# Performance work log

Measured on AMD Instinct MI355X. Metric: run time of the kernel, lower is better.

Reference implementation:

```python
import jax, jax.numpy as jnp
import numpy as np

# irreps layout: 256x0e (dim 256) + 128x1o (dim 384) + 64x2e (dim 320) -> total 960
MULS = (256, 128, 64)
DIMS = (1, 3, 5)  # 2l+1 for l = 0, 1, 2


def setup_inputs() -> dict:
    key = jax.random.key(0)
    k0, k1, k2, k3 = jax.random.split(key, 4)
    N = 131072
    total = sum(m * d for m, d in zip(MULS, DIMS))  # 960
    return {
        "features": jax.random.normal(k0, (N, total), dtype=jnp.float32),
        "w0": jax.random.normal(k1, (256, 256), dtype=jnp.float32),
        "w1": jax.random.normal(k2, (128, 128), dtype=jnp.float32),
        "w2": jax.random.normal(k3, (64, 64), dtype=jnp.float32),
    }


def _linear_irreps(features, weights):
    # Equivariant Linear == block-diagonal per-irrep matmul over the multiplicity
    # axis, broadcast over the (2l+1) m-components, scaled by 1/sqrt(mul_in)
    # (the net of e3nn's path_weight sqrt((2l+1)/mul_in) and the w3j 1/sqrt(2l+1)).
    outs = []
    off = 0
    for w, mul, d in zip(weights, MULS, DIMS):
        x = features[:, off:off + mul * d].reshape(-1, mul, d)  # [N, u, i]
        scale = 1.0 / np.sqrt(mul).astype(np.float32)
        y = jnp.einsum('zui,uw->zwi', x, w) * scale  # [N, w, i]
        outs.append(y.reshape(y.shape[0], mul * d))
        off += mul * d
    return jnp.concatenate(outs, axis=-1)  # [N, 960]


def reference(features, w0, w1, w2):
    return _linear_irreps(features, (w0, w1, w2))
```

## Files before the change

### kernel.cpp

```cpp
#include <hip/hip_runtime.h>

typedef short bf16x8 __attribute__((ext_vector_type(8)));
typedef float f32x4 __attribute__((ext_vector_type(4)));

__device__ __forceinline__ unsigned short f2bf(float f) {
    union { float f; unsigned u; } a;
    a.f = f;
    unsigned u = a.u;
    u += 0x7fffu + ((u >> 16) & 1u);
    return (unsigned short)(u >> 16);
}

__global__ void convert_w(const float* __restrict__ w, unsigned short* __restrict__ wt,
                          int mul, float scale) {
    int idx = blockIdx.x * blockDim.x + threadIdx.x;
    if (idx >= mul * mul) return;
    int n = idx / mul;
    int k = idx % mul;
    wt[idx] = f2bf(w[k * mul + n] * scale);
}

template<int MUL, int D, int OFF, int GM, int GN>
__global__ __launch_bounds__(256)
void irreps_linear(const float* __restrict__ x, const unsigned short* __restrict__ wt,
                   float* __restrict__ out) {
    constexpr int BM     = 32;
    constexpr int MP     = BM * D;
    constexpr int MT     = MP / 16;
    constexpr int NTL    = MUL / 16;
    constexpr int WM     = MT / GM;
    constexpr int WN     = NTL / GN;
    constexpr int LDA    = MUL + 8;
    constexpr int KSTEPS = MUL / 32;
    constexpr int REG    = MUL * D;
    constexpr int W4     = REG / 4;
    constexpr int LDC    = MUL + 1;
    constexpr int ABYTES = MP * LDA * 2;
    constexpr int CBYTES = (D > 1) ? MP * LDC * 4 : 0;
    constexpr int SBYTES = ABYTES > CBYTES ? ABYTES : CBYTES;

    __shared__ __align__(16) char smem[SBYTES];
    unsigned short* As = (unsigned short*)smem;

    const int  tid = threadIdx.x;
    const long z0  = (long)blockIdx.x * BM;
    const float* xr   = x   + z0 * 960 + OFF;
    float*       orow = out + z0 * 960 + OFF;

    #pragma unroll
    for (int it = 0; it < (BM * W4) / 256; ++it) {
        int idx = tid + it * 256;
        int zl  = idx / W4;
        int c4  = (idx % W4) * 4;
        f32x4 v = *(const f32x4*)(xr + (long)zl * 960 + c4);
        #pragma unroll
        for (int e = 0; e < 4; ++e) {
            int c = c4 + e;
            As[(zl * D + (c % D)) * LDA + (c / D)] = f2bf(v[e]);
        }
    }
    __syncthreads();

    const int lane = tid & 63;
    const int wv   = tid >> 6;
    const int wm0  = (wv / GN) * WM;
    const int wn0  = (wv % GN) * WN;
    const int lr   = lane & 15;
    const int lk   = (lane >> 4) * 8;

    f32x4 acc[WM][WN] = {};
    #pragma unroll
    for (int ks = 0; ks < KSTEPS; ++ks) {
        const int k0 = ks * 32 + lk;
        bf16x8 bfr[WN];
        #pragma unroll
        for (int in = 0; in < WN; ++in)
            bfr[in] = *(const bf16x8*)(wt + ((wn0 + in) * 16 + lr) * MUL + k0);
        #pragma unroll
        for (int im = 0; im < WM; ++im) {
            bf16x8 afr = *(const bf16x8*)(As + ((wm0 + im) * 16 + lr) * LDA + k0);
            #pragma unroll
            for (int in = 0; in < WN; ++in)
                acc[im][in] = __builtin_amdgcn_mfma_f32_16x16x32_bf16(
                    afr, bfr[in], acc[im][in], 0, 0, 0);
        }
    }

    if constexpr (D == 1) {
        #pragma unroll
        for (int im = 0; im < WM; ++im) {
            #pragma unroll
            for (int in = 0; in < WN; ++in) {
                int n  = (wn0 + in) * 16 + lr;
                int mb = (wm0 + im) * 16 + (lane >> 4) * 4;
                #pragma unroll
                for (int j = 0; j < 4; ++j)
                    orow[(long)(mb + j) * 960 + n] = acc[im][in][j];
            }
        }
    } else {
        __syncthreads();
        float* Cs = (float*)smem;
        #pragma unroll
        for (int im = 0; im < WM; ++im) {
            #pragma unroll
            for (int in = 0; in < WN; ++in) {
                int n  = (wn0 + in) * 16 + lr;
                int mb = (wm0 + im) * 16 + (lane >> 4) * 4;
                #pragma unroll
                for (int j = 0; j < 4; ++j)
                    Cs[(mb + j) * LDC + n] = acc[im][in][j];
            }
        }
        __syncthreads();
        #pragma unroll
        for (int it = 0; it < (BM * W4) / 256; ++it) {
            int idx = tid + it * 256;
            int zl  = idx / W4;
            int c4  = (idx % W4) * 4;
            f32x4 v;
            #pragma unroll
            for (int e = 0; e < 4; ++e) {
                int c = c4 + e;
                v[e] = Cs[(zl * D + (c % D)) * LDC + (c / D)];
            }
            *(f32x4*)(orow + (long)zl * 960 + c4) = v;
        }
    }
}

extern "C" void kernel_launch(void* const* d_in, const int* in_sizes, int n_in,
                              void* d_out, int out_size, void* d_ws, size_t ws_size,
                              hipStream_t stream) {
    const float* x  = (const float*)d_in[0];
    const float* w0 = (const float*)d_in[1];
    const float* w1 = (const float*)d_in[2];
    const float* w2 = (const float*)d_in[3];
    float* out = (float*)d_out;
    unsigned short* wt = (unsigned short*)d_ws;

    const int N  = in_sizes[0] / 960;
    const int nb = N / 32;

    convert_w<<<(256 * 256) / 256, 256, 0, stream>>>(w0, wt,         256, 0.0625f);
    convert_w<<<(128 * 128) / 256, 256, 0, stream>>>(w1, wt + 65536, 128, 0.08838834764831845f);
    convert_w<<<( 64 *  64) / 256, 256, 0, stream>>>(w2, wt + 81920,  64, 0.125f);

    irreps_linear<256, 1,   0, 1, 4><<<nb, 256, 0, stream>>>(x, wt,         out);
    irreps_linear<128, 3, 256, 2, 2><<<nb, 256, 0, stream>>>(x, wt + 65536, out);
    irreps_linear< 64, 5, 640, 2, 2><<<nb, 256, 0, stream>>>(x, wt + 81920, out);
}
```

Before: 307.9 us.

## Fuse three per-irrep GEMM kernels into one kernel over full rows

Replaces the three separate per-irrep kernel launches with one 512-thread kernel. Each block loads a full contiguous 960-float row tile once, scatters it into three bf16 LDS tiles, runs all three MFMA GEMMs, and writes the outputs back through LDS staged in sequence. This removes the extra launches and turns the strided partial-row reads into fully contiguous loads. In exchange it needs about 66KB of LDS and more syncs per block, which limits occupancy.

```diff
diff --git a/kernel.cpp b/kernel.cpp
--- a/kernel.cpp
+++ b/kernel.cpp
@@ -9,6 +9,10 @@
     unsigned u = a.u;
     u += 0x7fffu + ((u >> 16) & 1u);
     return (unsigned short)(u >> 16);
+}
+
+__device__ __forceinline__ f32x4 mfma16(bf16x8 a, bf16x8 b, f32x4 c) {
+    return __builtin_amdgcn_mfma_f32_16x16x32_bf16(a, b, c, 0, 0, 0);
 }
 
 __global__ void convert_w(const float* __restrict__ w, unsigned short* __restrict__ wt,
@@ -20,112 +24,167 @@
     wt[idx] = f2bf(w[k * mul + n] * scale);
 }
 
-template<int MUL, int D, int OFF, int GM, int GN>
-__global__ __launch_bounds__(256)
-void irreps_linear(const float* __restrict__ x, const unsigned short* __restrict__ wt,
-                   float* __restrict__ out) {
-    constexpr int BM     = 32;
-    constexpr int MP     = BM * D;
-    constexpr int MT     = MP / 16;
-    constexpr int NTL    = MUL / 16;
-    constexpr int WM     = MT / GM;
-    constexpr int WN     = NTL / GN;
-    constexpr int LDA    = MUL + 8;
-    constexpr int KSTEPS = MUL / 32;
-    constexpr int REG    = MUL * D;
-    constexpr int W4     = REG / 4;
-    constexpr int LDC    = MUL + 1;
-    constexpr int ABYTES = MP * LDA * 2;
-    constexpr int CBYTES = (D > 1) ? MP * LDC * 4 : 0;
-    constexpr int SBYTES = ABYTES > CBYTES ? ABYTES : CBYTES;
-
-    __shared__ __align__(16) char smem[SBYTES];
-    unsigned short* As = (unsigned short*)smem;
+__global__ __launch_bounds__(512, 4)
+void fused_linear(const float* __restrict__ x, const unsigned short* __restrict__ wt,
+                  float* __restrict__ out) {
+    __shared__ __align__(16) char smem[66048];
+    unsigned short* As0 = (unsigned short*)smem;
+    unsigned short* As1 = As0 + 32 * 264;
+    unsigned short* As2 = As1 + 96 * 136;
+    float* Cs = (float*)smem;
 
     const int  tid = threadIdx.x;
-    const long z0  = (long)blockIdx.x * BM;
-    const float* xr   = x   + z0 * 960 + OFF;
-    float*       orow = out + z0 * 960 + OFF;
-
-    #pragma unroll
-    for (int it = 0; it < (BM * W4) / 256; ++it) {
-        int idx = tid + it * 256;
-        int zl  = idx / W4;
-        int c4  = (idx % W4) * 4;
-        f32x4 v = *(const f32x4*)(xr + (long)zl * 960 + c4);
+    const long z0  = (long)blockIdx.x * 32;
+    const float* xr   = x   + z0 * 960;
+    float*       orow = out + z0 * 960;
+
+    #pragma unroll
+    for (int it = 0; it < 15; ++it) {
+        int idx = tid + it * 512;
+        f32x4 v = *(const f32x4*)(xr + (long)idx * 4);
+        int zl = idx / 240;
+        int c4 = (idx % 240) * 4;
         #pragma unroll
         for (int e = 0; e < 4; ++e) {
             int c = c4 + e;
-            As[(zl * D + (c % D)) * LDA + (c / D)] = f2bf(v[e]);
+            unsigned short b = f2bf(v[e]);
+            if (c < 256) {
+                As0[zl * 264 + c] = b;
+            } else if (c < 640) {
+                int cc = c - 256;
+                As1[(zl * 3 + cc % 3) * 136 + cc / 3] = b;
+            } else {
+                int cc = c - 640;
+                As2[(zl * 5 + cc % 5) * 72 + cc / 5] = b;
+            }
         }
     }
     __syncthreads();
 
     const int lane = tid & 63;
     const int wv   = tid >> 6;
-    const int wm0  = (wv / GN) * WM;
-    const int wn0  = (wv % GN) * WN;
     const int lr   = lane & 15;
-    const int lk   = (lane >> 4) * 8;
-
-    f32x4 acc[WM][WN] = {};
-    #pragma unroll
-    for (int ks = 0; ks < KSTEPS; ++ks) {
-        const int k0 = ks * 32 + lk;
-        bf16x8 bfr[WN];
-        #pragma unroll
-        for (int in = 0; in < WN; ++in)
-            bfr[in] = *(const bf16x8*)(wt + ((wn0 + in) * 16 + lr) * MUL + k0);
-        #pragma unroll
-        for (int im = 0; im < WM; ++im) {
-            bf16x8 afr = *(const bf16x8*)(As + ((wm0 + im) * 16 + lr) * LDA + k0);
-            #pragma unroll
-            for (int in = 0; in < WN; ++in)
-                acc[im][in] = __builtin_amdgcn_mfma_f32_16x16x32_bf16(
-                    afr, bfr[in], acc[im][in], 0, 0, 0);
-        }
-    }
-
-    if constexpr (D == 1) {
-        #pragma unroll
-        for (int im = 0; im < WM; ++im) {
-            #pragma unroll
-            for (int in = 0; in < WN; ++in) {
-                int n  = (wn0 + in) * 16 + lr;
-                int mb = (wm0 + im) * 16 + (lane >> 4) * 4;
-                #pragma unroll
-                for (int j = 0; j < 4; ++j)
-                    orow[(long)(mb + j) * 960 + n] = acc[im][in][j];
-            }
-        }
-    } else {
-        __syncthreads();
-        float* Cs = (float*)smem;
-        #pragma unroll
-        for (int im = 0; im < WM; ++im) {
-            #pragma unroll
-            for (int in = 0; in < WN; ++in) {
-                int n  = (wn0 + in) * 16 + lr;
-                int mb = (wm0 + im) * 16 + (lane >> 4) * 4;
-                #pragma unroll
-                for (int j = 0; j < 4; ++j)
-                    Cs[(mb + j) * LDC + n] = acc[im][in][j];
-            }
-        }
-        __syncthreads();
-        #pragma unroll
-        for (int it = 0; it < (BM * W4) / 256; ++it) {
-            int idx = tid + it * 256;
-            int zl  = idx / W4;
-            int c4  = (idx % W4) * 4;
-            f32x4 v;
-            #pragma unroll
-            for (int e = 0; e < 4; ++e) {
-                int c = c4 + e;
-                v[e] = Cs[(zl * D + (c % D)) * LDC + (c / D)];
-            }
-            *(f32x4*)(orow + (long)zl * 960 + c4) = v;
-        }
+    const int q    = lane >> 4;
+    const int lk   = q * 8;
+
+    f32x4 acc0[2][2] = {};
+    {
+        const unsigned short* w0 = wt;
+        #pragma unroll
+        for (int ks = 0; ks < 8; ++ks) {
+            int k0 = ks * 32 + lk;
+            bf16x8 b0 = *(const bf16x8*)(w0 + ((wv * 2 + 0) * 16 + lr) * 256 + k0);
+            bf16x8 b1 = *(const bf16x8*)(w0 + ((wv * 2 + 1) * 16 + lr) * 256 + k0);
+            #pragma unroll
+            for (int im = 0; im < 2; ++im) {
+                bf16x8 a = *(const bf16x8*)(As0 + (im * 16 + lr) * 264 + k0);
+                acc0[im][0] = mfma16(a, b0, acc0[im][0]);
+                acc0[im][1] = mfma16(a, b1, acc0[im][1]);
+            }
+        }
+    }
+
+    const int r1 = wv >> 2, c1 = wv & 3;
+    f32x4 acc1[3][2] = {};
+    {
+        const unsigned short* w1 = wt + 65536;
+        #pragma unroll
+        for (int ks = 0; ks < 4; ++ks) {
+            int k0 = ks * 32 + lk;
+            bf16x8 b0 = *(const bf16x8*)(w1 + ((c1 * 2 + 0) * 16 + lr) * 128 + k0);
+            bf16x8 b1 = *(const bf16x8*)(w1 + ((c1 * 2 + 1) * 16 + lr) * 128 + k0);
+            #pragma unroll
+            for (int im = 0; im < 3; ++im) {
+                bf16x8 a = *(const bf16x8*)(As1 + ((r1 * 3 + im) * 16 + lr) * 136 + k0);
+                acc1[im][0] = mfma16(a, b0, acc1[im][0]);
+                acc1[im][1] = mfma16(a, b1, acc1[im][1]);
+            }
+        }
+    }
+
+    f32x4 acc2[5] = {};
+    {
+        const unsigned short* w2 = wt + 81920;
+        #pragma unroll
+        for (int ks = 0; ks < 2; ++ks) {
+            int k0 = ks * 32 + lk;
+            bf16x8 b0 = *(const bf16x8*)(w2 + (c1 * 16 + lr) * 64 + k0);
+            #pragma unroll
+            for (int im = 0; im < 5; ++im) {
+                bf16x8 a = *(const bf16x8*)(As2 + ((r1 * 5 + im) * 16 + lr) * 72 + k0);
+                acc2[im] = mfma16(a, b0, acc2[im]);
+            }
+        }
+    }
+    __syncthreads();
+
+    #pragma unroll
+    for (int im = 0; im < 2; ++im)
+        #pragma unroll
+        for (int in = 0; in < 2; ++in) {
+            int col = (wv * 2 + in) * 16 + lr;
+            int row = im * 16 + q * 4;
+            #pragma unroll
+            for (int j = 0; j < 4; ++j)
+                Cs[(row + j) * 257 + col] = acc0[im][in][j];
+        }
+    __syncthreads();
+    #pragma unroll
+    for (int it = 0; it < 4; ++it) {
+        int idx = tid + it * 512;
+        int zl = idx / 64, c4 = (idx % 64) * 4;
+        f32x4 v;
+        #pragma unroll
+        for (int e = 0; e < 4; ++e) v[e] = Cs[zl * 257 + c4 + e];
+        *(f32x4*)(orow + (long)zl * 960 + c4) = v;
+    }
+    __syncthreads();
+
+    #pragma unroll
+    for (int im = 0; im < 3; ++im)
+        #pragma unroll
+        for (int in = 0; in < 2; ++in) {
+            int col = (c1 * 2 + in) * 16 + lr;
+            int row = (r1 * 3 + im) * 16 + q * 4;
+            #pragma unroll
+            for (int j = 0; j < 4; ++j)
+                Cs[(row + j) * 129 + col] = acc1[im][in][j];
+        }
+    __syncthreads();
+    #pragma unroll
+    for (int it = 0; it < 6; ++it) {
+        int idx = tid + it * 512;
+        int zl = idx / 96, c4 = (idx % 96) * 4;
+        f32x4 v;
+        #pragma unroll
+        for (int e = 0; e < 4; ++e) {
+            int c = c4 + e;
+            v[e] = Cs[(zl * 3 + c % 3) * 129 + c / 3];
+        }
+        *(f32x4*)(orow + (long)zl * 960 + 256 + c4) = v;
+    }
+    __syncthreads();
+
+    #pragma unroll
+    for (int im = 0; im < 5; ++im) {
+        int col = c1 * 16 + lr;
+        int row = (r1 * 5 + im) * 16 + q * 4;
+        #pragma unroll
+        for (int j = 0; j < 4; ++j)
+            Cs[(row + j) * 65 + col] = acc2[im][j];
+    }
+    __syncthreads();
+    #pragma unroll
+    for (int it = 0; it < 5; ++it) {
+        int idx = tid + it * 512;
+        int zl = idx / 80, c4 = (idx % 80) * 4;
+        f32x4 v;
+        #pragma unroll
+        for (int e = 0; e < 4; ++e) {
+            int c = c4 + e;
+            v[e] = Cs[(zl * 5 + c % 5) * 65 + c / 5];
+        }
+        *(f32x4*)(orow + (long)zl * 960 + 640 + c4) = v;
     }
 }
 
@@ -146,7 +205,5 @@
     convert_w<<<(128 * 128) / 256, 256, 0, stream>>>(w1, wt + 65536, 128, 0.08838834764831845f);
     convert_w<<<( 64 *  64) / 256, 256, 0, stream>>>(w2, wt + 81920,  64, 0.125f);
 
-    irreps_linear<256, 1,   0, 1, 4><<<nb, 256, 0, stream>>>(x, wt,         out);
-    irreps_linear<128, 3, 256, 2, 2><<<nb, 256, 0, stream>>>(x, wt + 65536, out);
-    irreps_linear< 64, 5, 640, 2, 2><<<nb, 256, 0, stream>>>(x, wt + 81920, out);
-}
+    fused_linear<<<nb, 512, 0, stream>>>(x, wt, out);
+}
```

After: 296.7 us. -3.7%, faster.

## Fuse irreps into one kernel using Kronecker-expanded block-diagonal weights

Applied to the files above, without the earlier changes.

Expands each l>0 weight into a dense (mul*D)x(mul*D) matrix that is zero except where the m-components match. This lets the input be loaded contiguously without the per-component transpose through shared memory. All three irreps are then processed in a single 512-thread kernel over 64-row tiles, replacing three launches. The trade-off is extra wasted MFMA work: about three times the FLOPs for l=1 and five times for l=2. Weight reads from global memory also grow.

```diff
diff --git a/kernel.cpp b/kernel.cpp
--- a/kernel.cpp
+++ b/kernel.cpp
@@ -4,129 +4,115 @@
 typedef float f32x4 __attribute__((ext_vector_type(4)));
 
 __device__ __forceinline__ unsigned short f2bf(float f) {
-    union { float f; unsigned u; } a;
-    a.f = f;
+    union { float f; unsigned u; } a; a.f = f;
     unsigned u = a.u;
     u += 0x7fffu + ((u >> 16) & 1u);
     return (unsigned short)(u >> 16);
 }
 
-__global__ void convert_w(const float* __restrict__ w, unsigned short* __restrict__ wt,
-                          int mul, float scale) {
-    int idx = blockIdx.x * blockDim.x + threadIdx.x;
-    if (idx >= mul * mul) return;
-    int n = idx / mul;
-    int k = idx % mul;
-    wt[idx] = f2bf(w[k * mul + n] * scale);
+__device__ __forceinline__ f32x4 mfma16(bf16x8 a, bf16x8 b, f32x4 c) {
+    return __builtin_amdgcn_mfma_f32_16x16x32_bf16(a, b, c, 0, 0, 0);
 }
 
-template<int MUL, int D, int OFF, int GM, int GN>
-__global__ __launch_bounds__(256)
-void irreps_linear(const float* __restrict__ x, const unsigned short* __restrict__ wt,
-                   float* __restrict__ out) {
-    constexpr int BM     = 32;
-    constexpr int MP     = BM * D;
-    constexpr int MT     = MP / 16;
-    constexpr int NTL    = MUL / 16;
-    constexpr int WM     = MT / GM;
-    constexpr int WN     = NTL / GN;
-    constexpr int LDA    = MUL + 8;
-    constexpr int KSTEPS = MUL / 32;
-    constexpr int REG    = MUL * D;
-    constexpr int W4     = REG / 4;
-    constexpr int LDC    = MUL + 1;
-    constexpr int ABYTES = MP * LDA * 2;
-    constexpr int CBYTES = (D > 1) ? MP * LDC * 4 : 0;
-    constexpr int SBYTES = ABYTES > CBYTES ? ABYTES : CBYTES;
+template<int D, int MUL>
+__global__ void expand_w(const float* __restrict__ w, unsigned short* __restrict__ wt,
+                         float scale) {
+    const int n = blockIdx.x;
+    const int k = threadIdx.x;
+    float v = 0.0f;
+    if (D == 1 || (n % D) == (k % D))
+        v = w[(k / D) * MUL + (n / D)] * scale;
+    wt[n * (MUL * D) + k] = f2bf(v);
+}
 
-    __shared__ __align__(16) char smem[SBYTES];
-    unsigned short* As = (unsigned short*)smem;
-
-    const int  tid = threadIdx.x;
-    const long z0  = (long)blockIdx.x * BM;
-    const float* xr   = x   + z0 * 960 + OFF;
-    float*       orow = out + z0 * 960 + OFF;
+template<int KP, int OFF, int BASE, bool TAIL>
+__device__ __forceinline__ void do_block(const float* __restrict__ xr,
+                                         const unsigned short* __restrict__ wb,
+                                         float* __restrict__ orow,
+                                         unsigned short* As,
+                                         int tid, int wv, int lr, int q) {
+    constexpr int P     = KP + 8;
+    constexpr int KS    = KP / 32;
+    constexpr int C8    = KP / 8;
+    constexpr int ITERS = KP / 64;
+    constexpr int NTW   = TAIL ? 3 : BASE;
 
     #pragma unroll
-    for (int it = 0; it < (BM * W4) / 256; ++it) {
-        int idx = tid + it * 256;
-        int zl  = idx / W4;
-        int c4  = (idx % W4) * 4;
-        f32x4 v = *(const f32x4*)(xr + (long)zl * 960 + c4);
-        #pragma unroll
-        for (int e = 0; e < 4; ++e) {
-            int c = c4 + e;
-            As[(zl * D + (c % D)) * LDA + (c / D)] = f2bf(v[e]);
-        }
+    for (int it = 0; it < ITERS; ++it) {
+        int idx = tid + it * 512;
+        int zl  = idx / C8;
+        int c8  = (idx - zl * C8) * 8;
+        const float* p = xr + zl * 960 + OFF + c8;
+        f32x4 v0 = *(const f32x4*)p;
+        f32x4 v1 = *(const f32x4*)(p + 4);
+        bf16x8 sv;
+        sv[0] = f2bf(v0[0]); sv[1] = f2bf(v0[1]); sv[2] = f2bf(v0[2]); sv[3] = f2bf(v0[3]);
+        sv[4] = f2bf(v1[0]); sv[5] = f2bf(v1[1]); sv[6] = f2bf(v1[2]); sv[7] = f2bf(v1[3]);
+        *(bf16x8*)(As + zl * P + c8) = sv;
     }
     __syncthreads();
 
-    const int lane = tid & 63;
-    const int wv   = tid >> 6;
-    const int wm0  = (wv / GN) * WM;
-    const int wn0  = (wv % GN) * WN;
-    const int lr   = lane & 15;
-    const int lk   = (lane >> 4) * 8;
+    int nts[NTW];
+    #pragma unroll
+    for (int in = 0; in < NTW; ++in)
+        nts[in] = (!TAIL || in < 2) ? (wv * BASE + in) : (16 + wv);
+    const bool t3 = !TAIL || (wv < 4);
 
-    f32x4 acc[WM][WN] = {};
+    f32x4 acc[4][NTW];
     #pragma unroll
-    for (int ks = 0; ks < KSTEPS; ++ks) {
-        const int k0 = ks * 32 + lk;
-        bf16x8 bfr[WN];
+    for (int mt = 0; mt < 4; ++mt)
         #pragma unroll
-        for (int in = 0; in < WN; ++in)
-            bfr[in] = *(const bf16x8*)(wt + ((wn0 + in) * 16 + lr) * MUL + k0);
+        for (int in = 0; in < NTW; ++in)
+            acc[mt][in] = (f32x4){0.f, 0.f, 0.f, 0.f};
+
+    #pragma unroll
+    for (int ks = 0; ks < KS; ++ks) {
+        const int kb = ks * 32 + q * 8;
+        bf16x8 b[NTW];
         #pragma unroll
-        for (int im = 0; im < WM; ++im) {
-            bf16x8 afr = *(const bf16x8*)(As + ((wm0 + im) * 16 + lr) * LDA + k0);
+        for (int in = 0; in < NTW; ++in)
+            if (in < 2 || t3)
+                b[in] = *(const bf16x8*)(wb + (nts[in] * 16 + lr) * KP + kb);
+        #pragma unroll
+        for (int mt = 0; mt < 4; ++mt) {
+            bf16x8 a = *(const bf16x8*)(As + (mt * 16 + lr) * P + kb);
             #pragma unroll
-            for (int in = 0; in < WN; ++in)
-                acc[im][in] = __builtin_amdgcn_mfma_f32_16x16x32_bf16(
-                    afr, bfr[in], acc[im][in], 0, 0, 0);
+            for (int in = 0; in < NTW; ++in)
+                if (in < 2 || t3)
+                    acc[mt][in] = mfma16(a, b[in], acc[mt][in]);
         }
     }
 
-    if constexpr (D == 1) {
+    #pragma unroll
+    for (int mt = 0; mt < 4; ++mt)
         #pragma unroll
-        for (int im = 0; im < WM; ++im) {
-            #pragma unroll
-            for (int in = 0; in < WN; ++in) {
-                int n  = (wn0 + in) * 16 + lr;
-                int mb = (wm0 + im) * 16 + (lane >> 4) * 4;
+        for (int in = 0; in < NTW; ++in)
+            if (in < 2 || t3) {
+                const int col = OFF + nts[in] * 16 + lr;
                 #pragma unroll
                 for (int j = 0; j < 4; ++j)
-                    orow[(long)(mb + j) * 960 + n] = acc[im][in][j];
+                    orow[(mt * 16 + q * 4 + j) * 960 + col] = acc[mt][in][j];
             }
-        }
-    } else {
-        __syncthreads();
-        float* Cs = (float*)smem;
-        #pragma unroll
-        for (int im = 0; im < WM; ++im) {
-            #pragma unroll
-            for (int in = 0; in < WN; ++in) {
-                int n  = (wn0 + in) * 16 + lr;
-                int mb = (wm0 + im) * 16 + (lane >> 4) * 4;
-                #pragma unroll
-                for (int j = 0; j < 4; ++j)
-                    Cs[(mb + j) * LDC + n] = acc[im][in][j];
-            }
-        }
-        __syncthreads();
-        #pragma unroll
-        for (int it = 0; it < (BM * W4) / 256; ++it) {
-            int idx = tid + it * 256;
-            int zl  = idx / W4;
-            int c4  = (idx % W4) * 4;
-            f32x4 v;
-            #pragma unroll
-            for (int e = 0; e < 4; ++e) {
-                int c = c4 + e;
-                v[e] = Cs[(zl * D + (c % D)) * LDC + (c / D)];
-            }
-            *(f32x4*)(orow + (long)zl * 960 + c4) = v;
-        }
-    }
+}
+
+__global__ __launch_bounds__(512, 4)
+void fused_linear(const float* __restrict__ x, const unsigned short* __restrict__ wt,
+                  float* __restrict__ out) {
+    __shared__ __align__(16) unsigned short As[64 * 392];
+    const int tid  = threadIdx.x;
+    const int lane = tid & 63;
+    const int wv   = tid >> 6;
+    const int lr   = lane & 15;
+    const int q    = lane >> 4;
+    const long z0  = (long)blockIdx.x * 64;
+    const float* xr = x + z0 * 960;
+    float* orow = out + z0 * 960;
+
+    do_block<256,   0, 2, false>(xr, wt,          orow, As, tid, wv, lr, q);
+    __syncthreads();
+    do_block<384, 256, 3, false>(xr, wt +  65536, orow, As, tid, wv, lr, q);
+    __syncthreads();
+    do_block<320, 640, 2, true >(xr, wt + 212992, orow, As, tid, wv, lr, q);
 }
 
 extern "C" void kernel_launch(void* const* d_in, const int* in_sizes, int n_in,
@@ -139,14 +125,11 @@
     float* out = (float*)d_out;
     unsigned short* wt = (unsigned short*)d_ws;
 
-    const int N  = in_sizes[0] / 960;
-    const int nb = N / 32;
+    const int N = in_sizes[0] / 960;
 
-    convert_w<<<(256 * 256) / 256, 256, 0, stream>>>(w0, wt,         256, 0.0625f);
-    convert_w<<<(128 * 128) / 256, 256, 0, stream>>>(w1, wt + 65536, 128, 0.08838834764831845f);
-    convert_w<<<( 64 *  64) / 256, 256, 0, stream>>>(w2, wt + 81920,  64, 0.125f);
+    expand_w<1, 256><<<256, 256, 0, stream>>>(w0, wt,          0.0625f);
+    expand_w<3, 128><<<384, 384, 0, stream>>>(w1, wt +  65536, 0.08838834764831845f);
+    expand_w<5,  64><<<320, 320, 0, stream>>>(w2, wt + 212992, 0.125f);
 
-    irreps_linear<256, 1,   0, 1, 4><<<nb, 256, 0, stream>>>(x, wt,         out);
-    irreps_linear<128, 3, 256, 2, 2><<<nb, 256, 0, stream>>>(x, wt + 65536, out);
-    irreps_linear< 64, 5, 640, 2, 2><<<nb, 256, 0, stream>>>(x, wt + 81920, out);
+    fused_linear<<<N / 64, 512, 0, stream>>>(x, wt, out);
 }
```

New measurement: 325.8 us. +5.8%, slower.
